# Performance work log

Measured on AMD Instinct MI355X. Metric: run time of the kernel, lower is better.

Reference implementation:

```python
import jax, jax.numpy as jnp
import numpy as np

B, S, D, H = 4, 2048, 1024, 16
DEPTH = D // H


def setup_inputs() -> dict:
    key = jax.random.key(0)
    ks = jax.random.split(key, 11)
    s = 1.0 / np.sqrt(D)
    return {
        "q": jax.random.normal(ks[0], (B, S, D), jnp.float32),
        "k": jax.random.normal(ks[1], (B, S, D), jnp.float32),
        "v": jax.random.normal(ks[2], (B, S, D), jnp.float32),
        "wq": jax.random.normal(ks[3], (D, D), jnp.float32) * s,
        "bq": jnp.zeros((D,), jnp.float32),
        "wk": jax.random.normal(ks[4], (D, D), jnp.float32) * s,
        "bk": jnp.zeros((D,), jnp.float32),
        "wv": jax.random.normal(ks[5], (D, D), jnp.float32) * s,
        "bv": jnp.zeros((D,), jnp.float32),
        "wo": jax.random.normal(ks[6], (D, D), jnp.float32) * s,
        "bo": jnp.zeros((D,), jnp.float32),
    }


def _split_heads(x):
    # [B,S,D] -> [B,H,S,depth]
    b, s, _ = x.shape
    return x.reshape(b, s, H, DEPTH).transpose(0, 2, 1, 3)


def reference(q, k, v, wq, bq, wk, bk, wv, bv, wo, bo):
    qh = _split_heads(q @ wq + bq)
    kh = _split_heads(k @ wk + bk)
    vh = _split_heads(v @ wv + bv)
    scale = 1.0 / jnp.sqrt(jnp.asarray(DEPTH, jnp.float32))
    logits = jnp.einsum("bhsd,bhtd->bhst", qh, kh) * scale  # [B,H,S,S]
    attn = jax.nn.softmax(logits, axis=-1)
    out = jnp.einsum("bhst,bhtd->bhsd", attn, vh)
    out = out.transpose(0, 2, 1, 3).reshape(q.shape[0], -1, D)
    return out @ wo + bo
```

## Files before the change

kernel.cpp:

```cpp
#include <hip/hip_runtime.h>
#include <hip/hip_bf16.h>

#define BATCH 4
#define SEQ   2048
#define DIM   1024
#define NHEAD 16
#define HDIM  64

typedef __bf16    bf16x8 __attribute__((ext_vector_type(8)));
typedef float     f32x16 __attribute__((ext_vector_type(16)));
typedef unsigned  u32;

__device__ __forceinline__ unsigned short f2bfu(float x) {
  union { __hip_bfloat16 b; unsigned short u; } c; c.b = __float2bfloat16(x); return c.u;
}
__device__ __forceinline__ u32 cvtpk(float lo, float hi) {
  u32 r; asm("v_cvt_pk_bf16_f32 %0, %1, %2" : "=v"(r) : "v"(lo), "v"(hi)); return r;
}
__device__ __forceinline__ int swz4(int row) {
  return ((row & 7) ^ ((row >> 3) & 7)) << 2;
}

#define GLDS16(GP, LP)                                                         \
  __builtin_amdgcn_global_load_lds(                                            \
      (const __attribute__((address_space(1))) void*)(GP),                     \
      (__attribute__((address_space(3))) void*)(LP), 16, 0, 0)

__global__ __launch_bounds__(256)
void wtrans(const float* __restrict__ w0, const float* __restrict__ w1,
            const float* __restrict__ w2,
            __hip_bfloat16* __restrict__ t0, __hip_bfloat16* __restrict__ t1,
            __hip_bfloat16* __restrict__ t2)
{
  __shared__ float T[64][68];
  const int mat  = blockIdx.x >> 8;
  const int tile = blockIdx.x & 255;
  const float* W = mat == 0 ? w0 : (mat == 1 ? w1 : w2);
  __hip_bfloat16* Wt = mat == 0 ? t0 : (mat == 1 ? t1 : t2);
  const int k0 = (tile >> 4) * 64, n0 = (tile & 15) * 64;
  const int tid = threadIdx.x;
  const int r = tid >> 2, cq = (tid & 3) * 16;
  #pragma unroll
  for (int j = 0; j < 4; ++j) {
    const float4 v = *reinterpret_cast<const float4*>(&W[(size_t)(k0 + r) * DIM + n0 + cq + j * 4]);
    T[r][cq + j * 4 + 0] = v.x; T[r][cq + j * 4 + 1] = v.y;
    T[r][cq + j * 4 + 2] = v.z; T[r][cq + j * 4 + 3] = v.w;
  }
  __syncthreads();
  u32 o[8];
  #pragma unroll
  for (int j = 0; j < 8; ++j)
    o[j] = cvtpk(T[cq + 2 * j][r], T[cq + 2 * j + 1][r]);
  *reinterpret_cast<uint4*>(&Wt[(size_t)(n0 + r) * DIM + k0 + cq + 0]) = make_uint4(o[0], o[1], o[2], o[3]);
  *reinterpret_cast<uint4*>(&Wt[(size_t)(n0 + r) * DIM + k0 + cq + 8]) = make_uint4(o[4], o[5], o[6], o[7]);
}

template<typename TIN, typename TOUT, int NSEG>
__global__ __launch_bounds__(256, 2)
void gemm_glds(const TIN* __restrict__ A0, const TIN* __restrict__ A1, const TIN* __restrict__ A2,
               const __hip_bfloat16* __restrict__ W0, const __hip_bfloat16* __restrict__ W1,
               const __hip_bfloat16* __restrict__ W2,
               const float* __restrict__ b0, const float* __restrict__ b1, const float* __restrict__ b2,
               TOUT* __restrict__ C0, TOUT* __restrict__ C1, TOUT* __restrict__ C2)
{
  extern __shared__ char smem[];
  constexpr bool AF32 = (sizeof(TIN) == 4);
  constexpr int ABYTES = 128 * 64 * sizeof(TIN);
  constexpr int K = 1024;

  const int seg = (NSEG == 1) ? 0 : (blockIdx.x >> 9);
  const int idb = (NSEG == 1) ? blockIdx.x : (blockIdx.x & 511);
  const TIN* A = seg == 0 ? A0 : (seg == 1 ? A1 : A2);
  const __hip_bfloat16* Wt = seg == 0 ? W0 : (seg == 1 ? W1 : W2);
  const float* bias = seg == 0 ? b0 : (seg == 1 ? b1 : b2);
  TOUT* C = seg == 0 ? C0 : (seg == 1 ? C1 : C2);

  const int xcd = idb & 7, rr = idb >> 3;
  const int bx = rr & 7, by = xcd + 8 * (rr >> 3);
  const int m0 = by * 128, n0 = bx * 128;

  const int tid = threadIdx.x, lane = tid & 63, w = tid >> 6;
  const int l31 = lane & 31, hi = lane >> 5;
  const int wm = w >> 1, wn = w & 1;

  f32x16 acc[2][2] = {};

  constexpr int NA = AF32 ? 8 : 4;
  const TIN* aptr[NA];
  #pragma unroll
  for (int i = 0; i < NA; ++i) {
    if constexpr (AF32) {
      const int off = (w * 8 + i) * 1024 + lane * 16;
      const int r = off >> 8;
      const int s = (off >> 4) & 15;
      const int e2 = ((r & 7) << 1) | ((r >> 3) & 1);
      aptr[i] = A + (size_t)(m0 + r) * K + (s ^ e2) * 4;
    } else {
      const int off = (w * 4 + i) * 1024 + lane * 16;
      const int r = off >> 7;
      const int s = (off >> 4) & 7;
      aptr[i] = A + (size_t)(m0 + r) * K + (s ^ (r & 7)) * 8;
    }
  }
  const __hip_bfloat16* bptr[4];
  #pragma unroll
  for (int i = 0; i < 4; ++i) {
    const int off = (w * 4 + i) * 1024 + lane * 16;
    const int r = off >> 7;
    const int s = (off >> 4) & 7;
    bptr[i] = Wt + (size_t)(n0 + r) * K + (s ^ (r & 7)) * 8;
  }

  int aoff[4][2], boff[4][2];
  #pragma unroll
  for (int kk = 0; kk < 4; ++kk) {
    #pragma unroll
    for (int mi = 0; mi < 2; ++mi) {
      const int r = wm * 64 + mi * 32 + l31;
      if constexpr (AF32) {
        const int e2 = ((r & 7) << 1) | ((r >> 3) & 1);
        aoff[kk][mi] = r * 256 + (((kk * 4 + hi * 2) ^ e2) << 4);
      } else {
        aoff[kk][mi] = r * 128 + (((kk * 2 + hi) ^ (r & 7)) << 4);
      }
    }
    #pragma unroll
    for (int ni = 0; ni < 2; ++ni) {
      const int c = wn * 64 + ni * 32 + l31;
      boff[kk][ni] = c * 128 + (((kk * 2 + hi) ^ (c & 7)) << 4);
    }
  }

  for (int t = 0; t < 16; ++t) {
    #pragma unroll
    for (int i = 0; i < NA; ++i) {
      GLDS16(aptr[i], smem + (w * NA + i) * 1024);
      aptr[i] += 64;
    }
    #pragma unroll
    for (int i = 0; i < 4; ++i) {
      GLDS16(bptr[i], smem + ABYTES + (w * 4 + i) * 1024);
      bptr[i] += 64;
    }
    __syncthreads();

    #pragma unroll
    for (int kk = 0; kk < 4; ++kk) {
      bf16x8 af[2], bfv[2];
      #pragma unroll
      for (int mi = 0; mi < 2; ++mi) {
        if constexpr (AF32) {
          const float4 f0 = *reinterpret_cast<const float4*>(smem + aoff[kk][mi]);
          const float4 f1 = *reinterpret_cast<const float4*>(smem + (aoff[kk][mi] ^ 16));
          union { u32 u[4]; bf16x8 v; } uu;
          uu.u[0] = cvtpk(f0.x, f0.y); uu.u[1] = cvtpk(f0.z, f0.w);
          uu.u[2] = cvtpk(f1.x, f1.y); uu.u[3] = cvtpk(f1.z, f1.w);
          af[mi] = uu.v;
        } else {
          af[mi] = *reinterpret_cast<const bf16x8*>(smem + aoff[kk][mi]);
        }
      }
      #pragma unroll
      for (int ni = 0; ni < 2; ++ni)
        bfv[ni] = *reinterpret_cast<const bf16x8*>(smem + ABYTES + boff[kk][ni]);
      __builtin_amdgcn_s_setprio(1);
      #pragma unroll
      for (int mi = 0; mi < 2; ++mi)
        #pragma unroll
        for (int ni = 0; ni < 2; ++ni)
          acc[mi][ni] = __builtin_amdgcn_mfma_f32_32x32x16_bf16(af[mi], bfv[ni], acc[mi][ni], 0, 0, 0);
      __builtin_amdgcn_s_setprio(0);
    }
    __syncthreads();
  }

  #pragma unroll
  for (int ni = 0; ni < 2; ++ni) {
    const int col = n0 + wn * 64 + ni * 32 + l31;
    const float bv = bias[col];
    #pragma unroll
    for (int mi = 0; mi < 2; ++mi) {
      #pragma unroll
      for (int g = 0; g < 4; ++g)
        #pragma unroll
        for (int e = 0; e < 4; ++e) {
          const int row = m0 + wm * 64 + mi * 32 + g * 8 + hi * 4 + e;
          const float val = acc[mi][ni][g * 4 + e] + bv;
          if constexpr (sizeof(TOUT) == 2)
            C[(size_t)row * DIM + col] = __float2bfloat16(val);
          else
            C[(size_t)row * DIM + col] = val;
        }
    }
  }
}

__global__ __launch_bounds__(256, 2)
void flash_attn(const __hip_bfloat16* __restrict__ Qb,
                const __hip_bfloat16* __restrict__ Kb,
                const __hip_bfloat16* __restrict__ Vb,
                __hip_bfloat16* __restrict__ Ob)
{
  __shared__ __align__(16) u32 Ks32[2][64][32];
  __shared__ __align__(16) u32 Vt32[2][64][32];

  const int id  = blockIdx.x;
  const int xcd = id & 7;
  const int r_  = id >> 3;
  const int qb  = r_ & 7;
  const int hh  = (r_ >> 3) & 1;
  const int b   = r_ >> 4;
  const int h   = xcd + 8 * hh;

  const int tid = threadIdx.x, lane = tid & 63, wv = tid >> 6;
  const int l31 = lane & 31, hi = lane >> 5;

  const size_t headoff = (size_t)h * HDIM;
  const int q0 = b * SEQ + qb * 256 + wv * 64;

  bf16x8 qf[2][4];
  #pragma unroll
  for (int qh = 0; qh < 2; ++qh)
    #pragma unroll
    for (int dk = 0; dk < 4; ++dk)
      qf[qh][dk] = *reinterpret_cast<const bf16x8*>(
        &Qb[(size_t)(q0 + qh * 32 + l31) * DIM + headoff + dk * 16 + hi * 8]);

  f32x16 accO[2][2] = {};
  float l_run[2] = {0.f, 0.f};

  const int skey = tid >> 2;
  const int sdq  = tid & 3;
  const int vkp  = tid >> 3;
  const int vdb  = tid & 7;
  const size_t kbase = (size_t)b * SEQ * DIM + headoff;

  uint4 kst[2], vst[2];
  auto load_t = [&](int t) {
    const int kb = t * 64;
    const __hip_bfloat16* kp_ = &Kb[kbase + (size_t)(kb + skey) * DIM + sdq * 16];
    kst[0] = *reinterpret_cast<const uint4*>(kp_);
    kst[1] = *reinterpret_cast<const uint4*>(kp_ + 8);
    const __hip_bfloat16* vp_ = &Vb[kbase + (size_t)(kb + vkp * 2) * DIM + vdb * 8];
    vst[0] = *reinterpret_cast<const uint4*>(vp_);
    vst[1] = *reinterpret_cast<const uint4*>(vp_ + DIM);
  };
  auto store_t = [&](int bb) {
    const int sk = swz4(skey);
    *reinterpret_cast<uint4*>(&Ks32[bb][skey][(sdq * 8 + 0) ^ sk]) = kst[0];
    *reinterpret_cast<uint4*>(&Ks32[bb][skey][(sdq * 8 + 4) ^ sk]) = kst[1];
    const unsigned short* a  = (const unsigned short*)&vst[0];
    const unsigned short* bv = (const unsigned short*)&vst[1];
    #pragma unroll
    for (int j = 0; j < 8; ++j) {
      const int row = vdb * 8 + j;
      Vt32[bb][row][vkp ^ swz4(row)] = (u32)a[j] | ((u32)bv[j] << 16);
    }
  };

  load_t(0); store_t(0); __syncthreads();

  const float C1 = 0.125f * 1.44269504f;

  for (int t = 0; t < SEQ / 64; ++t) {
    const int bb = t & 1;
    if (t < SEQ / 64 - 1) load_t(t + 1);

    f32x16 sacc[2][2] = {};
    __builtin_amdgcn_s_setprio(1);
    #pragma unroll
    for (int kt = 0; kt < 2; ++kt) {
      const int row = kt * 32 + l31;
      const int sk = swz4(row);
      #pragma unroll
      for (int dk = 0; dk < 4; ++dk) {
        bf16x8 kf = *reinterpret_cast<const bf16x8*>(&Ks32[bb][row][(dk * 8 + hi * 4) ^ sk]);
        sacc[0][kt] = __builtin_amdgcn_mfma_f32_32x32x16_bf16(kf, qf[0][dk], sacc[0][kt], 0, 0, 0);
        sacc[1][kt] = __builtin_amdgcn_mfma_f32_32x32x16_bf16(kf, qf[1][dk], sacc[1][kt], 0, 0, 0);
      }
    }
    __builtin_amdgcn_s_setprio(0);

    u32 pf[2][4][4];
    #pragma unroll
    for (int qh = 0; qh < 2; ++qh) {
      #pragma unroll
      for (int kt = 0; kt < 2; ++kt)
        #pragma unroll
        for (int r2 = 0; r2 < 16; ++r2)
          sacc[qh][kt][r2] = __builtin_amdgcn_exp2f(sacc[qh][kt][r2] * C1);

      f32x16 ps = sacc[qh][0] + sacc[qh][1];
      float s8[8];
      #pragma unroll
      for (int i = 0; i < 8; ++i) s8[i] = ps[i] + ps[i + 8];
      float rs = ((s8[0] + s8[1]) + (s8[2] + s8[3])) + ((s8[4] + s8[5]) + (s8[6] + s8[7]));
      rs += __shfl_xor(rs, 32);
      l_run[qh] += rs;

#define MAKE_PF(DST, P, B) do {                                            \
      u32 x1 = cvtpk(P[B+0], P[B+1]);                                      \
      u32 y1 = cvtpk(P[B+4], P[B+5]);                                      \
      u32 x2 = cvtpk(P[B+2], P[B+3]);                                      \
      u32 y2 = cvtpk(P[B+6], P[B+7]);                                      \
      auto s1 = __builtin_amdgcn_permlane32_swap(x1, y1, false, false);    \
      auto s2 = __builtin_amdgcn_permlane32_swap(x2, y2, false, false);    \
      DST[0] = (u32)s1[0]; DST[1] = (u32)s2[0];                            \
      DST[2] = (u32)s1[1]; DST[3] = (u32)s2[1];                            \
    } while (0)
      MAKE_PF(pf[qh][0], sacc[qh][0], 0);
      MAKE_PF(pf[qh][1], sacc[qh][0], 8);
      MAKE_PF(pf[qh][2], sacc[qh][1], 0);
      MAKE_PF(pf[qh][3], sacc[qh][1], 8);
#undef MAKE_PF
    }

    __builtin_amdgcn_s_setprio(1);
    #pragma unroll
    for (int dt = 0; dt < 2; ++dt) {
      const int row = dt * 32 + l31;
      const int sk = swz4(row);
      #pragma unroll
      for (int kf = 0; kf < 4; ++kf) {
        bf16x8 vf = *reinterpret_cast<const bf16x8*>(&Vt32[bb][row][(kf * 8 + hi * 4) ^ sk]);
        #pragma unroll
        for (int qh = 0; qh < 2; ++qh) {
          union { u32 u[4]; bf16x8 v; } pu;
          pu.u[0] = pf[qh][kf][0]; pu.u[1] = pf[qh][kf][1];
          pu.u[2] = pf[qh][kf][2]; pu.u[3] = pf[qh][kf][3];
          accO[qh][dt] = __builtin_amdgcn_mfma_f32_32x32x16_bf16(vf, pu.v, accO[qh][dt], 0, 0, 0);
        }
      }
    }
    __builtin_amdgcn_s_setprio(0);

    if (t < SEQ / 64 - 1) store_t(bb ^ 1);
    __syncthreads();
  }

  #pragma unroll
  for (int qh = 0; qh < 2; ++qh) {
    const float inv = 1.f / l_run[qh];
    const size_t rowbase = (size_t)(q0 + qh * 32 + l31) * DIM + headoff;
    #pragma unroll
    for (int dt = 0; dt < 2; ++dt)
      #pragma unroll
      for (int g = 0; g < 4; ++g) {
        ushort4 o;
        o.x = f2bfu(accO[qh][dt][g * 4 + 0] * inv);
        o.y = f2bfu(accO[qh][dt][g * 4 + 1] * inv);
        o.z = f2bfu(accO[qh][dt][g * 4 + 2] * inv);
        o.w = f2bfu(accO[qh][dt][g * 4 + 3] * inv);
        *reinterpret_cast<ushort4*>(&Ob[rowbase + dt * 32 + g * 8 + hi * 4]) = o;
      }
  }
}

extern "C" void kernel_launch(void* const* d_in, const int* in_sizes, int n_in,
                              void* d_out, int out_size, void* d_ws, size_t ws_size,
                              hipStream_t stream)
{
  const float* q  = (const float*)d_in[0];
  const float* k  = (const float*)d_in[1];
  const float* v  = (const float*)d_in[2];
  const float* wq = (const float*)d_in[3];
  const float* bq = (const float*)d_in[4];
  const float* wk = (const float*)d_in[5];
  const float* bk = (const float*)d_in[6];
  const float* wv = (const float*)d_in[7];
  const float* bv = (const float*)d_in[8];
  const float* wo = (const float*)d_in[9];
  const float* bo = (const float*)d_in[10];

  const size_t MN = (size_t)BATCH * SEQ * DIM;
  const size_t KK = (size_t)DIM * DIM;

  __hip_bfloat16* Qb = (__hip_bfloat16*)d_ws;
  __hip_bfloat16* Kb = Qb + MN;
  __hip_bfloat16* Vb = Kb + MN;
  __hip_bfloat16* S3 = Vb + MN;
  __hip_bfloat16* WtQ = S3;
  __hip_bfloat16* WtK = S3 + KK;
  __hip_bfloat16* WtV = S3 + 2 * KK;
  __hip_bfloat16* Ob  = S3;
  __hip_bfloat16* WtO = (__hip_bfloat16*)d_ws;

  wtrans<<<768, 256, 0, stream>>>(wq, wk, wv, WtQ, WtK, WtV);

  gemm_glds<float, __hip_bfloat16, 3><<<1536, 256, 49152, stream>>>(
      q, k, v, WtQ, WtK, WtV, bq, bk, bv, Qb, Kb, Vb);

  flash_attn<<<512, 256, 0, stream>>>(Qb, Kb, Vb, Ob);

  wtrans<<<256, 256, 0, stream>>>(wo, wo, wo, WtO, WtO, WtO);

  gemm_glds<__hip_bfloat16, float, 1><<<512, 256, 32768, stream>>>(
      Ob, Ob, Ob, WtO, WtO, WtO, bo, bo, bo,
      (float*)d_out, (float*)d_out, (float*)d_out);
}
```

Before: 202.9 us.

## Double-buffer GEMM tiles and convert fp32 A to bf16 before LDS staging

The projection GEMM becomes a two-stage pipeline with double-buffered LDS. The global loads for the next K-tile are issued before the MFMA work on the current tile, so there is one barrier per iteration instead of two. For fp32 activations, A is now loaded into registers, converted to bf16 and written to swizzled LDS after compute, rather than staged as fp32 through direct global-to-LDS loads and converted on every fragment read. This halves the A LDS footprint and removes repeated conversions. In exchange it adds register pressure from the prefetched float4s, which matters under launch_bounds(256,2).

```diff
diff --git a/kernel.cpp b/kernel.cpp
--- a/kernel.cpp
+++ b/kernel.cpp
@@ -57,16 +57,17 @@
 
 template<typename TIN, typename TOUT, int NSEG>
 __global__ __launch_bounds__(256, 2)
-void gemm_glds(const TIN* __restrict__ A0, const TIN* __restrict__ A1, const TIN* __restrict__ A2,
-               const __hip_bfloat16* __restrict__ W0, const __hip_bfloat16* __restrict__ W1,
-               const __hip_bfloat16* __restrict__ W2,
-               const float* __restrict__ b0, const float* __restrict__ b1, const float* __restrict__ b2,
-               TOUT* __restrict__ C0, TOUT* __restrict__ C1, TOUT* __restrict__ C2)
+void gemm2ph(const TIN* __restrict__ A0, const TIN* __restrict__ A1, const TIN* __restrict__ A2,
+             const __hip_bfloat16* __restrict__ W0, const __hip_bfloat16* __restrict__ W1,
+             const __hip_bfloat16* __restrict__ W2,
+             const float* __restrict__ b0, const float* __restrict__ b1, const float* __restrict__ b2,
+             TOUT* __restrict__ C0, TOUT* __restrict__ C1, TOUT* __restrict__ C2)
 {
-  extern __shared__ char smem[];
+  __shared__ __align__(16) u32 As32[2][128][32];
+  __shared__ __align__(16) u32 Bs32[2][128][32];
+
   constexpr bool AF32 = (sizeof(TIN) == 4);
-  constexpr int ABYTES = 128 * 64 * sizeof(TIN);
-  constexpr int K = 1024;
+  constexpr int K = 1024, NT = 16;
 
   const int seg = (NSEG == 1) ? 0 : (blockIdx.x >> 9);
   const int idb = (NSEG == 1) ? blockIdx.x : (blockIdx.x & 511);
@@ -85,23 +86,6 @@
 
   f32x16 acc[2][2] = {};
 
-  constexpr int NA = AF32 ? 8 : 4;
-  const TIN* aptr[NA];
-  #pragma unroll
-  for (int i = 0; i < NA; ++i) {
-    if constexpr (AF32) {
-      const int off = (w * 8 + i) * 1024 + lane * 16;
-      const int r = off >> 8;
-      const int s = (off >> 4) & 15;
-      const int e2 = ((r & 7) << 1) | ((r >> 3) & 1);
-      aptr[i] = A + (size_t)(m0 + r) * K + (s ^ e2) * 4;
-    } else {
-      const int off = (w * 4 + i) * 1024 + lane * 16;
-      const int r = off >> 7;
-      const int s = (off >> 4) & 7;
-      aptr[i] = A + (size_t)(m0 + r) * K + (s ^ (r & 7)) * 8;
-    }
-  }
   const __hip_bfloat16* bptr[4];
   #pragma unroll
   for (int i = 0; i < 4; ++i) {
@@ -110,6 +94,55 @@
     const int s = (off >> 4) & 7;
     bptr[i] = Wt + (size_t)(n0 + r) * K + (s ^ (r & 7)) * 8;
   }
+  const TIN* aptr[4];
+  const int arow = tid >> 3;
+  const int acb  = (tid & 7) * 8;
+  #pragma unroll
+  for (int i = 0; i < 4; ++i) {
+    if constexpr (!AF32) {
+      const int off = (w * 4 + i) * 1024 + lane * 16;
+      const int r = off >> 7;
+      const int s = (off >> 4) & 7;
+      aptr[i] = A + (size_t)(m0 + r) * K + (s ^ (r & 7)) * 8;
+    } else {
+      aptr[i] = nullptr;
+    }
+  }
+
+  float4 ar[4][2];
+
+  auto loadA_f32 = [&](int t) {
+    #pragma unroll
+    for (int p = 0; p < 4; ++p) {
+      const float* ap = (const float*)A + (size_t)(m0 + arow + p * 32) * K + t * 64 + acb;
+      ar[p][0] = *reinterpret_cast<const float4*>(ap);
+      ar[p][1] = *reinterpret_cast<const float4*>(ap + 4);
+    }
+  };
+  auto writeA_f32 = [&](int nxt) {
+    #pragma unroll
+    for (int p = 0; p < 4; ++p) {
+      const int row = arow + p * 32;
+      uint4 pk;
+      pk.x = cvtpk(ar[p][0].x, ar[p][0].y);
+      pk.y = cvtpk(ar[p][0].z, ar[p][0].w);
+      pk.z = cvtpk(ar[p][1].x, ar[p][1].y);
+      pk.w = cvtpk(ar[p][1].z, ar[p][1].w);
+      *reinterpret_cast<uint4*>(&As32[nxt][row][((tid & 7) * 4) ^ ((row & 7) << 2)]) = pk;
+    }
+  };
+  auto stageA_bf = [&](int nxt, int t) {
+    #pragma unroll
+    for (int i = 0; i < 4; ++i)
+      GLDS16((const __hip_bfloat16*)aptr[i] + t * 64,
+             (char*)As32 + nxt * 16384 + (w * 4 + i) * 1024);
+  };
+  auto stageB = [&](int nxt, int t) {
+    #pragma unroll
+    for (int i = 0; i < 4; ++i)
+      GLDS16(bptr[i] + t * 64,
+             (char*)Bs32 + nxt * 16384 + (w * 4 + i) * 1024);
+  };
 
   int aoff[4][2], boff[4][2];
   #pragma unroll
@@ -117,12 +150,7 @@
     #pragma unroll
     for (int mi = 0; mi < 2; ++mi) {
       const int r = wm * 64 + mi * 32 + l31;
-      if constexpr (AF32) {
-        const int e2 = ((r & 7) << 1) | ((r >> 3) & 1);
-        aoff[kk][mi] = r * 256 + (((kk * 4 + hi * 2) ^ e2) << 4);
-      } else {
-        aoff[kk][mi] = r * 128 + (((kk * 2 + hi) ^ (r & 7)) << 4);
-      }
+      aoff[kk][mi] = r * 128 + (((kk * 2 + hi) ^ (r & 7)) << 4);
     }
     #pragma unroll
     for (int ni = 0; ni < 2; ++ni) {
@@ -131,38 +159,31 @@
     }
   }
 
-  for (int t = 0; t < 16; ++t) {
-    #pragma unroll
-    for (int i = 0; i < NA; ++i) {
-      GLDS16(aptr[i], smem + (w * NA + i) * 1024);
-      aptr[i] += 64;
-    }
-    #pragma unroll
-    for (int i = 0; i < 4; ++i) {
-      GLDS16(bptr[i], smem + ABYTES + (w * 4 + i) * 1024);
-      bptr[i] += 64;
-    }
-    __syncthreads();
-
+  if constexpr (AF32) { loadA_f32(0); writeA_f32(0); }
+  else                { stageA_bf(0, 0); }
+  stageB(0, 0);
+  __syncthreads();
+
+  for (int t = 0; t < NT; ++t) {
+    const int cur = t & 1, nxt = cur ^ 1;
+
+    if (t + 1 < NT) {
+      if constexpr (AF32) loadA_f32(t + 1);
+      else                stageA_bf(nxt, t + 1);
+      stageB(nxt, t + 1);
+    }
+
+    const char* ab = (const char*)As32 + cur * 16384;
+    const char* bb = (const char*)Bs32 + cur * 16384;
     #pragma unroll
     for (int kk = 0; kk < 4; ++kk) {
       bf16x8 af[2], bfv[2];
       #pragma unroll
-      for (int mi = 0; mi < 2; ++mi) {
-        if constexpr (AF32) {
-          const float4 f0 = *reinterpret_cast<const float4*>(smem + aoff[kk][mi]);
-          const float4 f1 = *reinterpret_cast<const float4*>(smem + (aoff[kk][mi] ^ 16));
-          union { u32 u[4]; bf16x8 v; } uu;
-          uu.u[0] = cvtpk(f0.x, f0.y); uu.u[1] = cvtpk(f0.z, f0.w);
-          uu.u[2] = cvtpk(f1.x, f1.y); uu.u[3] = cvtpk(f1.z, f1.w);
-          af[mi] = uu.v;
-        } else {
-          af[mi] = *reinterpret_cast<const bf16x8*>(smem + aoff[kk][mi]);
-        }
-      }
+      for (int mi = 0; mi < 2; ++mi)
+        af[mi] = *reinterpret_cast<const bf16x8*>(ab + aoff[kk][mi]);
       #pragma unroll
       for (int ni = 0; ni < 2; ++ni)
-        bfv[ni] = *reinterpret_cast<const bf16x8*>(smem + ABYTES + boff[kk][ni]);
+        bfv[ni] = *reinterpret_cast<const bf16x8*>(bb + boff[kk][ni]);
       __builtin_amdgcn_s_setprio(1);
       #pragma unroll
       for (int mi = 0; mi < 2; ++mi)
@@ -170,6 +191,10 @@
         for (int ni = 0; ni < 2; ++ni)
           acc[mi][ni] = __builtin_amdgcn_mfma_f32_32x32x16_bf16(af[mi], bfv[ni], acc[mi][ni], 0, 0, 0);
       __builtin_amdgcn_s_setprio(0);
+    }
+
+    if (t + 1 < NT) {
+      if constexpr (AF32) writeA_f32(nxt);
     }
     __syncthreads();
   }
@@ -387,14 +412,14 @@
 
   wtrans<<<768, 256, 0, stream>>>(wq, wk, wv, WtQ, WtK, WtV);
 
-  gemm_glds<float, __hip_bfloat16, 3><<<1536, 256, 49152, stream>>>(
+  gemm2ph<float, __hip_bfloat16, 3><<<1536, 256, 0, stream>>>(
       q, k, v, WtQ, WtK, WtV, bq, bk, bv, Qb, Kb, Vb);
 
   flash_attn<<<512, 256, 0, stream>>>(Qb, Kb, Vb, Ob);
 
   wtrans<<<256, 256, 0, stream>>>(wo, wo, wo, WtO, WtO, WtO);
 
-  gemm_glds<__hip_bfloat16, float, 1><<<512, 256, 32768, stream>>>(
+  gemm2ph<__hip_bfloat16, float, 1><<<512, 256, 0, stream>>>(
       Ob, Ob, Ob, WtO, WtO, WtO, bo, bo, bo,
       (float*)d_out, (float*)d_out, (float*)d_out);
 }
```

New measurement: 208.1 us. 2.6% more time.
